# Kernel optimization log

Measured on AMD Instinct MI355X. Metric: run time of the kernel, lower is better.

## Reference

```python
import jax, jax.numpy as jnp
import numpy as np

N_NODES = 50000
N_EDGES = 1600000
IN_CH = 128
HID = 128
OUT_CH = 2
N_GRAPHS = 512
N_HID_LAYERS = 5  # first 5 SAGEConv+BN+ReLU blocks; 6th conv has no BN/act
EPS = 1e-5


def setup_inputs() -> dict:
    key = jax.random.key(0)
    ks = jax.random.split(key, 13)
    x = jax.random.normal(ks[0], (N_NODES, IN_CH), jnp.float32)
    edge_index = jax.random.randint(ks[1], (2, N_EDGES), 0, N_NODES)
    batch = jnp.sort(jax.random.randint(ks[2], (N_NODES,), 0, N_GRAPHS))
    s = 1.0 / np.sqrt(HID)
    # SAGEConv params for the 5 hidden layers (in==hid==128 so they stack)
    Wl = jax.random.normal(ks[3], (N_HID_LAYERS, HID, HID), jnp.float32) * s  # lin_l (neighbors)
    Wr = jax.random.normal(ks[4], (N_HID_LAYERS, HID, HID), jnp.float32) * s  # lin_r (root)
    b = jax.random.normal(ks[5], (N_HID_LAYERS, HID), jnp.float32) * s
    # BatchNorm (eval mode: running stats + affine)
    gamma = 1.0 + 0.1 * jax.random.normal(ks[6], (N_HID_LAYERS, HID), jnp.float32)
    beta = 0.1 * jax.random.normal(ks[7], (N_HID_LAYERS, HID), jnp.float32)
    rmean = 0.1 * jax.random.normal(ks[8], (N_HID_LAYERS, HID), jnp.float32)
    rvar = 0.5 + jax.random.uniform(ks[9], (N_HID_LAYERS, HID), dtype=jnp.float32)
    # final SAGEConv: hid -> out
    Wl_out = jax.random.normal(ks[10], (HID, OUT_CH), jnp.float32) * s
    Wr_out = jax.random.normal(ks[11], (HID, OUT_CH), jnp.float32) * s
    b_out = jax.random.normal(ks[12], (OUT_CH,), jnp.float32) * s
    return dict(x=x, Wl=Wl, Wr=Wr, b=b, gamma=gamma, beta=beta, rmean=rmean,
                rvar=rvar, Wl_out=Wl_out, Wr_out=Wr_out, b_out=b_out,
                edge_index=edge_index, batch=batch)


def reference(x, Wl, Wr, b, gamma, beta, rmean, rvar, Wl_out, Wr_out, b_out,
              edge_index, batch):
    src, dst = edge_index[0], edge_index[1]
    # in-degree for mean aggregation (shared across all layers)
    deg = jax.ops.segment_sum(jnp.ones((src.shape[0],), x.dtype), dst,
                              num_segments=N_NODES)
    inv_deg = (1.0 / jnp.maximum(deg, 1.0))[:, None]  # [N,1]

    def sage(h, Wl_, Wr_, b_):
        # PyG SAGEConv: lin_l(mean_{j in N(i)} x_j) + lin_r(x_i)
        agg = jax.ops.segment_sum(h[src], dst, num_segments=N_NODES) * inv_deg
        return agg @ Wl_ + h @ Wr_ + b_

    h = x
    for l in range(N_HID_LAYERS):
        h = sage(h, Wl[l], Wr[l], b[l])
        # BatchNorm1d in eval mode: affine with running stats
        h = (h - rmean[l]) * (gamma[l] * jax.lax.rsqrt(rvar[l] + EPS)) + beta[l]
        h = jax.nn.relu(h)
        # F.dropout(p=0.2, training=False) is identity in eval
    h = sage(h, Wl_out, Wr_out, b_out)  # [N, OUT_CH]
    # global_mean_pool over graphs
    gsum = jax.ops.segment_sum(h, batch, num_segments=N_GRAPHS)
    gcnt = jax.ops.segment_sum(jnp.ones((h.shape[0],), h.dtype), batch,
                               num_segments=N_GRAPHS)
    return gsum / jnp.maximum(gcnt, 1.0)[:, None]  # [N_GRAPHS, OUT_CH]
```

## Files before the change

### kernel.cpp

```cpp
#include <hip/hip_runtime.h>

#define HID 128
#define BN_EPS 1e-5f

typedef short bf16x8 __attribute__((ext_vector_type(8)));
typedef float f32x4 __attribute__((ext_vector_type(4)));

__device__ inline unsigned short f2b(float f) {
  unsigned int u = __float_as_uint(f);
  unsigned int r = (u + 0x7fffu + ((u >> 16) & 1u)) >> 16;
  return (unsigned short)r;
}
__device__ inline float bl(unsigned int v) { return __uint_as_float(v << 16); }
__device__ inline float bh(unsigned int v) { return __uint_as_float(v & 0xffff0000u); }


__global__ void k_bhist(const int* __restrict__ dst, int* __restrict__ bcnt, int e, int nb) {
  __shared__ int h[256];
  for (int i = threadIdx.x; i < 256; i += blockDim.x) h[i] = 0;
  __syncthreads();
  int stride = gridDim.x * blockDim.x;
  for (int i = blockIdx.x * blockDim.x + threadIdx.x; i < e; i += stride)
    atomicAdd(&h[dst[i] >> 8], 1);
  __syncthreads();
  for (int i = threadIdx.x; i < nb; i += blockDim.x)
    if (h[i]) atomicAdd(&bcnt[i], h[i]);
}

__global__ void k_bscan(const int* __restrict__ bcnt, int* __restrict__ base,
                        int* __restrict__ cur, int nb) {
  __shared__ int ws[4];
  int t = threadIdx.x;
  int v = (t < nb) ? bcnt[t] : 0;
  int lane = t & 63, wid = t >> 6;
  int x = v;
#pragma unroll
  for (int off = 1; off < 64; off <<= 1) {
    int y = __shfl_up(x, off, 64);
    if (lane >= off) x += y;
  }
  if (lane == 63) ws[wid] = x;
  __syncthreads();
  int add = 0;
  for (int w = 0; w < wid; ++w) add += ws[w];
  int incl = x + add;
  int excl = incl - v;
  if (t < nb) { base[t] = excl; cur[t] = excl; }
  if (t == nb - 1) base[nb] = incl;
}

__global__ void k_bscatter(const int* __restrict__ src, const int* __restrict__ dst,
                           int* __restrict__ cur, unsigned int* __restrict__ binned, int e) {
  __shared__ int bc[256];
  __shared__ int bo[256];
  int nchunk = (e + gridDim.x - 1) / gridDim.x;
  int c0 = blockIdx.x * nchunk;
  int c1 = min(c0 + nchunk, e);
  for (int i = threadIdx.x; i < 256; i += blockDim.x) bc[i] = 0;
  __syncthreads();
  for (int i = c0 + threadIdx.x; i < c1; i += blockDim.x)
    atomicAdd(&bc[dst[i] >> 8], 1);
  __syncthreads();
  for (int i = threadIdx.x; i < 256; i += blockDim.x) {
    int c = bc[i];
    bo[i] = c ? atomicAdd(&cur[i], c) : 0;
    bc[i] = 0;
  }
  __syncthreads();
  for (int i = c0 + threadIdx.x; i < c1; i += blockDim.x) {
    int d = dst[i];
    int b = d >> 8;
    int pos = bo[b] + atomicAdd(&bc[b], 1);
    binned[pos] = (unsigned)src[i] | ((unsigned)(d & 255) << 16);
  }
}

__global__ __launch_bounds__(256) void k_bfill(
    const unsigned int* __restrict__ binned, const int* __restrict__ base,
    int* __restrict__ row_ptr, float* __restrict__ inv_deg,
    int* __restrict__ col, int n, int nb) {
  __shared__ int cnt[256];
  __shared__ int cur[256];
  __shared__ int ws[4];
  int b = blockIdx.x;
  int t = threadIdx.x;
  int n0 = b << 8;
  int e0 = base[b], e1 = base[b + 1];
  cnt[t] = 0;
  __syncthreads();
  for (int i = e0 + t; i < e1; i += 256)
    atomicAdd(&cnt[binned[i] >> 16], 1);
  __syncthreads();
  int v = cnt[t];
  int lane = t & 63, wid = t >> 6;
  int x = v;
#pragma unroll
  for (int off = 1; off < 64; off <<= 1) {
    int y = __shfl_up(x, off, 64);
    if (lane >= off) x += y;
  }
  if (lane == 63) ws[wid] = x;
  __syncthreads();
  int add = 0;
  for (int w = 0; w < wid; ++w) add += ws[w];
  int excl = x - v + add;
  int node = n0 + t;
  if (node < n) {
    row_ptr[node] = e0 + excl;
    inv_deg[node] = 1.0f / (float)max(v, 1);
  }
  cur[t] = e0 + excl;
  __syncthreads();
  for (int i = e0 + t; i < e1; i += 256) {
    unsigned int pr = binned[i];
    int pos = atomicAdd(&cur[pr >> 16], 1);
    col[pos] = (int)(pr & 0xffffu);
  }
  if (b == 0 && t == 0) row_ptr[n] = base[nb];
}


__global__ void k_prep(const float* __restrict__ x, unsigned short* __restrict__ xb,
                       const float* __restrict__ Wl, const float* __restrict__ Wr,
                       unsigned short* __restrict__ Wlt, unsigned short* __restrict__ Wrt,
                       const float* __restrict__ g, const float* __restrict__ be,
                       const float* __restrict__ rm, const float* __restrict__ rv,
                       float* __restrict__ sc, float* __restrict__ sh,
                       int n4, int wtot, int bn) {
  int i = blockIdx.x * blockDim.x + threadIdx.x;
  if (i < n4) {
    float4 v = ((const float4*)x)[i];
    unsigned int lo = (unsigned int)f2b(v.x) | ((unsigned int)f2b(v.y) << 16);
    unsigned int hi = (unsigned int)f2b(v.z) | ((unsigned int)f2b(v.w) << 16);
    ((uint2*)xb)[i] = make_uint2(lo, hi);
  } else if (i < n4 + wtot) {
    int j = i - n4;
    int mat = j >> 14, rem = j & 16383, nn = rem >> 7, kk = rem & 127;
    int sidx = (mat << 14) + (kk << 7) + nn;
    Wlt[j] = f2b(Wl[sidx]);
    Wrt[j] = f2b(Wr[sidx]);
  } else if (i < n4 + wtot + bn) {
    int j = i - n4 - wtot;
    float s = g[j] * rsqrtf(rv[j] + BN_EPS);
    sc[j] = s;
    sh[j] = be[j] - rm[j] * s;
  }
}


__global__ __launch_bounds__(128) void k_spmm_g(
    const unsigned short* __restrict__ hbsrc, const int* __restrict__ row_ptr,
    const int* __restrict__ col, const float* __restrict__ inv_deg,
    unsigned short* __restrict__ aggb, int n) {
  int node = blockIdx.x * 2 + (threadIdx.x >> 6);
  if (node >= n) return;
  int lane = threadIdx.x & 63;
  int slot = lane >> 4, c16 = lane & 15;
  int beg = row_ptr[node], end = row_ptr[node + 1];
  float a0 = 0, a1 = 0, a2 = 0, a3 = 0, a4 = 0, a5 = 0, a6 = 0, a7 = 0;
  const unsigned short* base = hbsrc + (c16 << 3);
  int e = beg;
  for (; e + 16 <= end; e += 16) {
    int s0 = col[e + slot];
    int s1 = col[e + 4 + slot];
    int s2 = col[e + 8 + slot];
    int s3 = col[e + 12 + slot];
    uint4 v0 = *(const uint4*)(base + ((size_t)s0 << 7));
    uint4 v1 = *(const uint4*)(base + ((size_t)s1 << 7));
    uint4 v2 = *(const uint4*)(base + ((size_t)s2 << 7));
    uint4 v3 = *(const uint4*)(base + ((size_t)s3 << 7));
    a0 += bl(v0.x); a1 += bh(v0.x); a2 += bl(v0.y); a3 += bh(v0.y);
    a4 += bl(v0.z); a5 += bh(v0.z); a6 += bl(v0.w); a7 += bh(v0.w);
    a0 += bl(v1.x); a1 += bh(v1.x); a2 += bl(v1.y); a3 += bh(v1.y);
    a4 += bl(v1.z); a5 += bh(v1.z); a6 += bl(v1.w); a7 += bh(v1.w);
    a0 += bl(v2.x); a1 += bh(v2.x); a2 += bl(v2.y); a3 += bh(v2.y);
    a4 += bl(v2.z); a5 += bh(v2.z); a6 += bl(v2.w); a7 += bh(v2.w);
    a0 += bl(v3.x); a1 += bh(v3.x); a2 += bl(v3.y); a3 += bh(v3.y);
    a4 += bl(v3.z); a5 += bh(v3.z); a6 += bl(v3.w); a7 += bh(v3.w);
  }
  for (; e < end; e += 4) {
    int idx = e + slot;
    if (idx < end) {
      int s = col[idx];
      uint4 v = *(const uint4*)(base + ((size_t)s << 7));
      a0 += bl(v.x); a1 += bh(v.x); a2 += bl(v.y); a3 += bh(v.y);
      a4 += bl(v.z); a5 += bh(v.z); a6 += bl(v.w); a7 += bh(v.w);
    }
  }
#pragma unroll
  for (int st = 16; st <= 32; st <<= 1) {
    a0 += __shfl_xor(a0, st); a1 += __shfl_xor(a1, st);
    a2 += __shfl_xor(a2, st); a3 += __shfl_xor(a3, st);
    a4 += __shfl_xor(a4, st); a5 += __shfl_xor(a5, st);
    a6 += __shfl_xor(a6, st); a7 += __shfl_xor(a7, st);
  }
  if (slot == 0) {
    float w = inv_deg[node];
    unsigned int p0 = (unsigned int)f2b(a0 * w) | ((unsigned int)f2b(a1 * w) << 16);
    unsigned int p1 = (unsigned int)f2b(a2 * w) | ((unsigned int)f2b(a3 * w) << 16);
    unsigned int p2 = (unsigned int)f2b(a4 * w) | ((unsigned int)f2b(a5 * w) << 16);
    unsigned int p3 = (unsigned int)f2b(a6 * w) | ((unsigned int)f2b(a7 * w) << 16);
    *(uint4*)(aggb + ((size_t)node << 7) + (c16 << 3)) = make_uint4(p0, p1, p2, p3);
  }
}


__global__ __launch_bounds__(256) void k_gemm3(
    const unsigned short* __restrict__ aggb,
    const unsigned short* __restrict__ hbsrc,
    const unsigned short* __restrict__ Wlt,
    const unsigned short* __restrict__ Wrt,
    const float* __restrict__ bias, const float* __restrict__ sc,
    const float* __restrict__ sh, unsigned short* __restrict__ hbo,
    int n, int ngroups) {
  int w = threadIdx.x >> 6;
  int lane = threadIdx.x & 63;
  int l15 = lane & 15, lhi = lane >> 4;

  bf16x8 aL[2][4], aR[2][4];
#pragma unroll
  for (int ms = 0; ms < 2; ++ms) {
    int row = (w << 5) + (ms << 4) + l15;
#pragma unroll
    for (int ks = 0; ks < 4; ++ks) {
      aL[ms][ks] = *(const bf16x8*)(Wlt + (row << 7) + (ks << 5) + (lhi << 3));
      aR[ms][ks] = *(const bf16x8*)(Wrt + (row << 7) + (ks << 5) + (lhi << 3));
    }
  }
  float4 bi[2], scv[2], shv[2];
#pragma unroll
  for (int ms = 0; ms < 2; ++ms) {
    int ch = (w << 5) + (ms << 4) + (lhi << 2);
    bi[ms] = *(const float4*)(bias + ch);
    scv[ms] = *(const float4*)(sc + ch);
    shv[ms] = *(const float4*)(sh + ch);
  }

  for (int g0 = blockIdx.x * 2; g0 < ngroups; g0 += gridDim.x * 2) {
    int g1 = g0 + 1;
    int nodeA = (g0 << 4) + l15;
    bool okA = nodeA < n;
    bool okB = (g1 < ngroups);
    int nodeB = okB ? (g1 << 4) + l15 : nodeA;
    okB = okB && nodeB < n;
    int nsA = okA ? nodeA : 0;
    int nsB = okB ? nodeB : 0;
    const unsigned short* arowA = aggb + ((size_t)nsA << 7) + (lhi << 3);
    const unsigned short* hrowA = hbsrc + ((size_t)nsA << 7) + (lhi << 3);
    const unsigned short* arowB = aggb + ((size_t)nsB << 7) + (lhi << 3);
    const unsigned short* hrowB = hbsrc + ((size_t)nsB << 7) + (lhi << 3);
    bf16x8 bA[4], bH[4], cA[4], cH[4];
#pragma unroll
    for (int ks = 0; ks < 4; ++ks) {
      bA[ks] = *(const bf16x8*)(arowA + (ks << 5));
      bH[ks] = *(const bf16x8*)(hrowA + (ks << 5));
      cA[ks] = *(const bf16x8*)(arowB + (ks << 5));
      cH[ks] = *(const bf16x8*)(hrowB + (ks << 5));
    }
    f32x4 acc0[2], acc1[2];
#pragma unroll
    for (int ms = 0; ms < 2; ++ms) { acc0[ms] = (f32x4)(0.f); acc1[ms] = (f32x4)(0.f); }
#pragma unroll
    for (int ms = 0; ms < 2; ++ms) {
#pragma unroll
      for (int ks = 0; ks < 4; ++ks) {
        acc0[ms] = __builtin_amdgcn_mfma_f32_16x16x32_bf16(aL[ms][ks], bA[ks], acc0[ms], 0, 0, 0);
        acc1[ms] = __builtin_amdgcn_mfma_f32_16x16x32_bf16(aL[ms][ks], cA[ks], acc1[ms], 0, 0, 0);
      }
#pragma unroll
      for (int ks = 0; ks < 4; ++ks) {
        acc0[ms] = __builtin_amdgcn_mfma_f32_16x16x32_bf16(aR[ms][ks], bH[ks], acc0[ms], 0, 0, 0);
        acc1[ms] = __builtin_amdgcn_mfma_f32_16x16x32_bf16(aR[ms][ks], cH[ks], acc1[ms], 0, 0, 0);
      }
    }
#pragma unroll
    for (int ms = 0; ms < 2; ++ms) {
      int ch = (w << 5) + (ms << 4) + (lhi << 2);
      if (okA) {
        float o0 = fmaxf((acc0[ms][0] + bi[ms].x) * scv[ms].x + shv[ms].x, 0.f);
        float o1 = fmaxf((acc0[ms][1] + bi[ms].y) * scv[ms].y + shv[ms].y, 0.f);
        float o2 = fmaxf((acc0[ms][2] + bi[ms].z) * scv[ms].z + shv[ms].z, 0.f);
        float o3 = fmaxf((acc0[ms][3] + bi[ms].w) * scv[ms].w + shv[ms].w, 0.f);
        unsigned int lo = (unsigned int)f2b(o0) | ((unsigned int)f2b(o1) << 16);
        unsigned int hi = (unsigned int)f2b(o2) | ((unsigned int)f2b(o3) << 16);
        *(uint2*)(hbo + ((size_t)nodeA << 7) + ch) = make_uint2(lo, hi);
      }
      if (okB) {
        float o0 = fmaxf((acc1[ms][0] + bi[ms].x) * scv[ms].x + shv[ms].x, 0.f);
        float o1 = fmaxf((acc1[ms][1] + bi[ms].y) * scv[ms].y + shv[ms].y, 0.f);
        float o2 = fmaxf((acc1[ms][2] + bi[ms].z) * scv[ms].z + shv[ms].z, 0.f);
        float o3 = fmaxf((acc1[ms][3] + bi[ms].w) * scv[ms].w + shv[ms].w, 0.f);
        unsigned int lo = (unsigned int)f2b(o0) | ((unsigned int)f2b(o1) << 16);
        unsigned int hi = (unsigned int)f2b(o2) | ((unsigned int)f2b(o3) << 16);
        *(uint2*)(hbo + ((size_t)nodeB << 7) + ch) = make_uint2(lo, hi);
      }
    }
  }
}


__global__ void k_pq(const unsigned short* __restrict__ hb, const float* __restrict__ Wl_out,
                     const float* __restrict__ Wr_out, float* __restrict__ p,
                     float* __restrict__ q, int n) {
  int node = blockIdx.x * 4 + (threadIdx.x >> 6);
  if (node >= n) return;
  int lane = threadIdx.x & 63;
  unsigned int hv = *(const unsigned int*)(hb + ((size_t)node << 7) + (lane << 1));
  float hx = bl(hv), hy = bh(hv);
  float4 wl = *(const float4*)(Wl_out + (lane << 2));
  float4 wr = *(const float4*)(Wr_out + (lane << 2));
  float p0 = hx * wl.x + hy * wl.z;
  float p1 = hx * wl.y + hy * wl.w;
  float q0 = hx * wr.x + hy * wr.z;
  float q1 = hx * wr.y + hy * wr.w;
#pragma unroll
  for (int off = 32; off > 0; off >>= 1) {
    p0 += __shfl_xor(p0, off, 64);
    p1 += __shfl_xor(p1, off, 64);
    q0 += __shfl_xor(q0, off, 64);
    q1 += __shfl_xor(q1, off, 64);
  }
  if (lane == 0) {
    *(float2*)(p + (size_t)node * 2) = make_float2(p0, p1);
    *(float2*)(q + (size_t)node * 2) = make_float2(q0, q1);
  }
}

__global__ void k_spmm2p(const float* __restrict__ p, const float* __restrict__ q,
                         const int* __restrict__ row_ptr, const int* __restrict__ col,
                         const float* __restrict__ inv_deg, const float* __restrict__ b_out,
                         const int* __restrict__ batch, float* __restrict__ out,
                         float* __restrict__ gcnt, int n) {
  int i = blockIdx.x * blockDim.x + threadIdx.x;
  int lane = threadIdx.x & 63;
  bool valid = i < n;
  float o0 = 0.f, o1 = 0.f;
  int g = -1;
  if (valid) {
    int beg = row_ptr[i], end = row_ptr[i + 1];
    float a0 = 0.f, a1 = 0.f, b0 = 0.f, b1 = 0.f;
    int e = beg;
    for (; e + 2 <= end; e += 2) {
      float2 v0 = *(const float2*)(p + (size_t)col[e] * 2);
      float2 v1 = *(const float2*)(p + (size_t)col[e + 1] * 2);
      a0 += v0.x; a1 += v0.y; b0 += v1.x; b1 += v1.y;
    }
    if (e < end) {
      float2 v = *(const float2*)(p + (size_t)col[e] * 2);
      a0 += v.x; a1 += v.y;
    }
    float w = inv_deg[i];
    float2 qv = *(const float2*)(q + (size_t)i * 2);
    o0 = (a0 + b0) * w + qv.x + b_out[0];
    o1 = (a1 + b1) * w + qv.y + b_out[1];
    g = batch[i];
  }
  float s0 = o0, s1 = o1;
#pragma unroll
  for (int off = 1; off < 64; off <<= 1) {
    float y0 = __shfl_up(s0, off, 64);
    float y1 = __shfl_up(s1, off, 64);
    if (lane >= off) { s0 += y0; s1 += y1; }
  }
  int gprev = __shfl_up(g, 1, 64);
  int gnext = __shfl_down(g, 1, 64);
  bool is_start = (lane == 0) || (g != gprev);
  bool is_end = valid && ((lane == 63) || (g != gnext));
  int startl = is_start ? lane : 0;
#pragma unroll
  for (int off = 1; off < 64; off <<= 1) {
    int y = __shfl_up(startl, off, 64);
    if (lane >= off) startl = max(startl, y);
  }
  int prevl = startl > 0 ? startl - 1 : 0;
  float t0 = __shfl(s0, prevl, 64);
  float t1 = __shfl(s1, prevl, 64);
  if (is_end) {
    float p0 = startl > 0 ? t0 : 0.f;
    float p1 = startl > 0 ? t1 : 0.f;
    atomicAdd(&out[g * 2], s0 - p0);
    atomicAdd(&out[g * 2 + 1], s1 - p1);
    atomicAdd(&gcnt[g], (float)(lane - startl + 1));
  }
}

__global__ void k_div(float* __restrict__ out, const float* __restrict__ gcnt, int ng) {
  int i = blockIdx.x * blockDim.x + threadIdx.x;
  if (i < ng * 2) out[i] /= fmaxf(gcnt[i >> 1], 1.0f);
}


extern "C" void kernel_launch(void* const* d_in, const int* in_sizes, int n_in,
                              void* d_out, int out_size, void* d_ws, size_t ws_size,
                              hipStream_t stream) {
  const float* x = (const float*)d_in[0];
  const float* Wl = (const float*)d_in[1];
  const float* Wr = (const float*)d_in[2];
  const float* b = (const float*)d_in[3];
  const float* gamma = (const float*)d_in[4];
  const float* beta = (const float*)d_in[5];
  const float* rmean = (const float*)d_in[6];
  const float* rvar = (const float*)d_in[7];
  const float* Wl_out = (const float*)d_in[8];
  const float* Wr_out = (const float*)d_in[9];
  const float* b_out = (const float*)d_in[10];
  const int* eidx = (const int*)d_in[11];
  const int* batch = (const int*)d_in[12];

  const int N = in_sizes[0] / HID;
  const int E = in_sizes[11] / 2;
  const int L = in_sizes[1] / (HID * HID);
  const int NG = out_size / 2;
  const int NB = (N + 255) >> 8;
  const int NGRP = (N + 15) >> 4;
  const int* src = eidx;
  const int* dst = eidx + E;

  char* ws = (char*)d_ws;
  size_t off = 0;
  auto alloc = [&](size_t bytes) {
    void* ptr = ws + off;
    off += (bytes + 255) & ~(size_t)255;
    return ptr;
  };
  int* row_ptr = (int*)alloc((size_t)(N + 1) * 4);
  int* bcnt = (int*)alloc((size_t)NB * 4);
  int* bbase = (int*)alloc((size_t)(NB + 1) * 4);
  int* bcur = (int*)alloc((size_t)NB * 4);
  int* col = (int*)alloc((size_t)E * 4);
  float* inv_deg = (float*)alloc((size_t)N * 4);
  unsigned short* xb = (unsigned short*)alloc((size_t)N * HID * 2);
  unsigned short* hb0 = (unsigned short*)alloc((size_t)N * HID * 2);
  unsigned short* hb1 = (unsigned short*)alloc((size_t)N * HID * 2);
  unsigned short* aggb = (unsigned short*)alloc((size_t)N * HID * 2);
  unsigned short* Wlt = (unsigned short*)alloc((size_t)L * HID * HID * 2);
  unsigned short* Wrt = (unsigned short*)alloc((size_t)L * HID * HID * 2);
  float* sc = (float*)alloc((size_t)L * HID * 4);
  float* sh = (float*)alloc((size_t)L * HID * 4);
  float* p = (float*)alloc((size_t)N * 2 * 4);
  float* q = (float*)alloc((size_t)N * 2 * 4);
  float* gcnt = (float*)alloc((size_t)NG * 4);
  unsigned int* binned = (unsigned int*)alloc((size_t)E * 4);

  hipMemsetAsync(bcnt, 0, (size_t)NB * 4, stream);
  k_bhist<<<256, 256, 0, stream>>>(dst, bcnt, E, NB);
  k_bscan<<<1, 256, 0, stream>>>(bcnt, bbase, bcur, NB);
  k_bscatter<<<256, 256, 0, stream>>>(src, dst, bcur, binned, E);
  k_bfill<<<NB, 256, 0, stream>>>(binned, bbase, row_ptr, inv_deg, col, N, NB);

  const int n4 = N * HID / 4;
  const int wtot = L * HID * HID;
  const int bn = L * HID;
  k_prep<<<(n4 + wtot + bn + 255) / 256, 256, 0, stream>>>(
      x, xb, Wl, Wr, Wlt, Wrt, gamma, beta, rmean, rvar, sc, sh, n4, wtot, bn);

  const unsigned short* hin = xb;
  for (int l = 0; l < L; ++l) {
    unsigned short* hnext = (l & 1) ? hb1 : hb0;
    k_spmm_g<<<(N + 1) / 2, 128, 0, stream>>>(hin, row_ptr, col, inv_deg, aggb, N);
    k_gemm3<<<512, 256, 0, stream>>>(
        aggb, hin, Wlt + (size_t)l * HID * HID, Wrt + (size_t)l * HID * HID,
        b + (size_t)l * HID, sc + (size_t)l * HID, sh + (size_t)l * HID,
        hnext, N, NGRP);
    hin = hnext;
  }
  k_pq<<<(N + 3) / 4, 256, 0, stream>>>(hin, Wl_out, Wr_out, p, q, N);
  hipMemsetAsync(d_out, 0, (size_t)out_size * 4, stream);
  hipMemsetAsync(gcnt, 0, (size_t)NG * 4, stream);
  k_spmm2p<<<(N + 255) / 256, 256, 0, stream>>>(
      p, q, row_ptr, col, inv_deg, b_out, batch, (float*)d_out, gcnt, N);
  k_div<<<(NG * 2 + 255) / 256, 256, 0, stream>>>((float*)d_out, gcnt, NG);
}
```

Before: 453.1 us.

## Split feature storage into four channel slices for cache-local gather

Stores node features as four planes of 32 channels each, and splits the SpMM gather across four blocks, one per slice. Each slice plane is 3.2 MB, so the randomly gathered working set per kernel pass can fit in L2/MALL better than the full 12.8 MB row-major array. The gather loop now handles 16 edges per iteration with 4 lanes per row, and uses nontemporal loads and stores for col and agg. In exchange, col/row_ptr is read four times and the block count quadruples. The GEMM and pq kernels are adjusted to the new layout.

```diff
diff --git a/kernel.cpp b/kernel.cpp
--- a/kernel.cpp
+++ b/kernel.cpp
@@ -5,6 +5,7 @@
 
 typedef short bf16x8 __attribute__((ext_vector_type(8)));
 typedef float f32x4 __attribute__((ext_vector_type(4)));
+typedef unsigned int u32x4 __attribute__((ext_vector_type(4)));
 
 __device__ inline unsigned short f2b(float f) {
   unsigned int u = __float_as_uint(f);
@@ -13,6 +14,7 @@
 }
 __device__ inline float bl(unsigned int v) { return __uint_as_float(v << 16); }
 __device__ inline float bh(unsigned int v) { return __uint_as_float(v & 0xffff0000u); }
+
 
 
 __global__ void k_bhist(const int* __restrict__ dst, int* __restrict__ bcnt, int e, int nb) {
@@ -126,13 +128,15 @@
                        const float* __restrict__ g, const float* __restrict__ be,
                        const float* __restrict__ rm, const float* __restrict__ rv,
                        float* __restrict__ sc, float* __restrict__ sh,
-                       int n4, int wtot, int bn) {
+                       int n4, int wtot, int bn, int ps) {
   int i = blockIdx.x * blockDim.x + threadIdx.x;
   if (i < n4) {
     float4 v = ((const float4*)x)[i];
     unsigned int lo = (unsigned int)f2b(v.x) | ((unsigned int)f2b(v.y) << 16);
     unsigned int hi = (unsigned int)f2b(v.z) | ((unsigned int)f2b(v.w) << 16);
-    ((uint2*)xb)[i] = make_uint2(lo, hi);
+    int flat = i << 2;
+    int node = flat >> 7, c = flat & 127;
+    *(uint2*)(xb + (size_t)(c >> 5) * ps + node * 32 + (c & 31)) = make_uint2(lo, hi);
   } else if (i < n4 + wtot) {
     int j = i - n4;
     int mat = j >> 14, rem = j & 16383, nn = rem >> 7, kk = rem & 127;
@@ -151,44 +155,34 @@
 __global__ __launch_bounds__(128) void k_spmm_g(
     const unsigned short* __restrict__ hbsrc, const int* __restrict__ row_ptr,
     const int* __restrict__ col, const float* __restrict__ inv_deg,
-    unsigned short* __restrict__ aggb, int n) {
-  int node = blockIdx.x * 2 + (threadIdx.x >> 6);
+    unsigned short* __restrict__ aggb, int n, int ps) {
+  int bid = blockIdx.x;
+  int slice = bid & 3;
+  int node = ((bid >> 2) << 1) + (threadIdx.x >> 6);
   if (node >= n) return;
   int lane = threadIdx.x & 63;
-  int slot = lane >> 4, c16 = lane & 15;
+  int slot = lane >> 2, c4 = lane & 3;
   int beg = row_ptr[node], end = row_ptr[node + 1];
+  const unsigned short* base = hbsrc + (size_t)slice * ps + (c4 << 3);
   float a0 = 0, a1 = 0, a2 = 0, a3 = 0, a4 = 0, a5 = 0, a6 = 0, a7 = 0;
-  const unsigned short* base = hbsrc + (c16 << 3);
   int e = beg;
   for (; e + 16 <= end; e += 16) {
-    int s0 = col[e + slot];
-    int s1 = col[e + 4 + slot];
-    int s2 = col[e + 8 + slot];
-    int s3 = col[e + 12 + slot];
-    uint4 v0 = *(const uint4*)(base + ((size_t)s0 << 7));
-    uint4 v1 = *(const uint4*)(base + ((size_t)s1 << 7));
-    uint4 v2 = *(const uint4*)(base + ((size_t)s2 << 7));
-    uint4 v3 = *(const uint4*)(base + ((size_t)s3 << 7));
-    a0 += bl(v0.x); a1 += bh(v0.x); a2 += bl(v0.y); a3 += bh(v0.y);
-    a4 += bl(v0.z); a5 += bh(v0.z); a6 += bl(v0.w); a7 += bh(v0.w);
-    a0 += bl(v1.x); a1 += bh(v1.x); a2 += bl(v1.y); a3 += bh(v1.y);
-    a4 += bl(v1.z); a5 += bh(v1.z); a6 += bl(v1.w); a7 += bh(v1.w);
-    a0 += bl(v2.x); a1 += bh(v2.x); a2 += bl(v2.y); a3 += bh(v2.y);
-    a4 += bl(v2.z); a5 += bh(v2.z); a6 += bl(v2.w); a7 += bh(v2.w);
-    a0 += bl(v3.x); a1 += bh(v3.x); a2 += bl(v3.y); a3 += bh(v3.y);
-    a4 += bl(v3.z); a5 += bh(v3.z); a6 += bl(v3.w); a7 += bh(v3.w);
-  }
-  for (; e < end; e += 4) {
+    int s = __builtin_nontemporal_load(&col[e + slot]);
+    uint4 v = *(const uint4*)(base + (size_t)s * 32);
+    a0 += bl(v.x); a1 += bh(v.x); a2 += bl(v.y); a3 += bh(v.y);
+    a4 += bl(v.z); a5 += bh(v.z); a6 += bl(v.w); a7 += bh(v.w);
+  }
+  if (e < end) {
     int idx = e + slot;
     if (idx < end) {
-      int s = col[idx];
-      uint4 v = *(const uint4*)(base + ((size_t)s << 7));
+      int s = __builtin_nontemporal_load(&col[idx]);
+      uint4 v = *(const uint4*)(base + (size_t)s * 32);
       a0 += bl(v.x); a1 += bh(v.x); a2 += bl(v.y); a3 += bh(v.y);
       a4 += bl(v.z); a5 += bh(v.z); a6 += bl(v.w); a7 += bh(v.w);
     }
   }
 #pragma unroll
-  for (int st = 16; st <= 32; st <<= 1) {
+  for (int st = 4; st <= 32; st <<= 1) {
     a0 += __shfl_xor(a0, st); a1 += __shfl_xor(a1, st);
     a2 += __shfl_xor(a2, st); a3 += __shfl_xor(a3, st);
     a4 += __shfl_xor(a4, st); a5 += __shfl_xor(a5, st);
@@ -196,11 +190,13 @@
   }
   if (slot == 0) {
     float w = inv_deg[node];
-    unsigned int p0 = (unsigned int)f2b(a0 * w) | ((unsigned int)f2b(a1 * w) << 16);
-    unsigned int p1 = (unsigned int)f2b(a2 * w) | ((unsigned int)f2b(a3 * w) << 16);
-    unsigned int p2 = (unsigned int)f2b(a4 * w) | ((unsigned int)f2b(a5 * w) << 16);
-    unsigned int p3 = (unsigned int)f2b(a6 * w) | ((unsigned int)f2b(a7 * w) << 16);
-    *(uint4*)(aggb + ((size_t)node << 7) + (c16 << 3)) = make_uint4(p0, p1, p2, p3);
+    u32x4 pk;
+    pk[0] = (unsigned int)f2b(a0 * w) | ((unsigned int)f2b(a1 * w) << 16);
+    pk[1] = (unsigned int)f2b(a2 * w) | ((unsigned int)f2b(a3 * w) << 16);
+    pk[2] = (unsigned int)f2b(a4 * w) | ((unsigned int)f2b(a5 * w) << 16);
+    pk[3] = (unsigned int)f2b(a6 * w) | ((unsigned int)f2b(a7 * w) << 16);
+    u32x4* dstp = (u32x4*)(aggb + (size_t)slice * ps + node * 32 + (c4 << 3));
+    __builtin_nontemporal_store(pk, dstp);
   }
 }
 
@@ -212,7 +208,7 @@
     const unsigned short* __restrict__ Wrt,
     const float* __restrict__ bias, const float* __restrict__ sc,
     const float* __restrict__ sh, unsigned short* __restrict__ hbo,
-    int n, int ngroups) {
+    int n, int ngroups, int ps) {
   int w = threadIdx.x >> 6;
   int lane = threadIdx.x & 63;
   int l15 = lane & 15, lhi = lane >> 4;
@@ -245,17 +241,14 @@
     okB = okB && nodeB < n;
     int nsA = okA ? nodeA : 0;
     int nsB = okB ? nodeB : 0;
-    const unsigned short* arowA = aggb + ((size_t)nsA << 7) + (lhi << 3);
-    const unsigned short* hrowA = hbsrc + ((size_t)nsA << 7) + (lhi << 3);
-    const unsigned short* arowB = aggb + ((size_t)nsB << 7) + (lhi << 3);
-    const unsigned short* hrowB = hbsrc + ((size_t)nsB << 7) + (lhi << 3);
     bf16x8 bA[4], bH[4], cA[4], cH[4];
 #pragma unroll
     for (int ks = 0; ks < 4; ++ks) {
-      bA[ks] = *(const bf16x8*)(arowA + (ks << 5));
-      bH[ks] = *(const bf16x8*)(hrowA + (ks << 5));
-      cA[ks] = *(const bf16x8*)(arowB + (ks << 5));
-      cH[ks] = *(const bf16x8*)(hrowB + (ks << 5));
+      size_t po = (size_t)ks * ps + (lhi << 3);
+      bA[ks] = *(const bf16x8*)(aggb + po + nsA * 32);
+      bH[ks] = *(const bf16x8*)(hbsrc + po + nsA * 32);
+      cA[ks] = *(const bf16x8*)(aggb + po + nsB * 32);
+      cH[ks] = *(const bf16x8*)(hbsrc + po + nsB * 32);
     }
     f32x4 acc0[2], acc1[2];
 #pragma unroll
@@ -275,7 +268,7 @@
     }
 #pragma unroll
     for (int ms = 0; ms < 2; ++ms) {
-      int ch = (w << 5) + (ms << 4) + (lhi << 2);
+      int choff = (ms << 4) + (lhi << 2);
       if (okA) {
         float o0 = fmaxf((acc0[ms][0] + bi[ms].x) * scv[ms].x + shv[ms].x, 0.f);
         float o1 = fmaxf((acc0[ms][1] + bi[ms].y) * scv[ms].y + shv[ms].y, 0.f);
@@ -283,7 +276,7 @@
         float o3 = fmaxf((acc0[ms][3] + bi[ms].w) * scv[ms].w + shv[ms].w, 0.f);
         unsigned int lo = (unsigned int)f2b(o0) | ((unsigned int)f2b(o1) << 16);
         unsigned int hi = (unsigned int)f2b(o2) | ((unsigned int)f2b(o3) << 16);
-        *(uint2*)(hbo + ((size_t)nodeA << 7) + ch) = make_uint2(lo, hi);
+        *(uint2*)(hbo + (size_t)w * ps + nodeA * 32 + choff) = make_uint2(lo, hi);
       }
       if (okB) {
         float o0 = fmaxf((acc1[ms][0] + bi[ms].x) * scv[ms].x + shv[ms].x, 0.f);
@@ -292,7 +285,7 @@
         float o3 = fmaxf((acc1[ms][3] + bi[ms].w) * scv[ms].w + shv[ms].w, 0.f);
         unsigned int lo = (unsigned int)f2b(o0) | ((unsigned int)f2b(o1) << 16);
         unsigned int hi = (unsigned int)f2b(o2) | ((unsigned int)f2b(o3) << 16);
-        *(uint2*)(hbo + ((size_t)nodeB << 7) + ch) = make_uint2(lo, hi);
+        *(uint2*)(hbo + (size_t)w * ps + nodeB * 32 + choff) = make_uint2(lo, hi);
       }
     }
   }
@@ -301,11 +294,12 @@
 
 __global__ void k_pq(const unsigned short* __restrict__ hb, const float* __restrict__ Wl_out,
                      const float* __restrict__ Wr_out, float* __restrict__ p,
-                     float* __restrict__ q, int n) {
+                     float* __restrict__ q, int n, int ps) {
   int node = blockIdx.x * 4 + (threadIdx.x >> 6);
   if (node >= n) return;
   int lane = threadIdx.x & 63;
-  unsigned int hv = *(const unsigned int*)(hb + ((size_t)node << 7) + (lane << 1));
+  int c = lane << 1;
+  unsigned int hv = *(const unsigned int*)(hb + (size_t)(c >> 5) * ps + node * 32 + (c & 31));
   float hx = bl(hv), hy = bh(hv);
   float4 wl = *(const float4*)(Wl_out + (lane << 2));
   float4 wr = *(const float4*)(Wr_out + (lane << 2));
@@ -413,6 +407,7 @@
   const int NG = out_size / 2;
   const int NB = (N + 255) >> 8;
   const int NGRP = (N + 15) >> 4;
+  const int PS = N * 32;
   const int* src = eidx;
   const int* dst = eidx + E;
 
@@ -452,19 +447,19 @@
   const int wtot = L * HID * HID;
   const int bn = L * HID;
   k_prep<<<(n4 + wtot + bn + 255) / 256, 256, 0, stream>>>(
-      x, xb, Wl, Wr, Wlt, Wrt, gamma, beta, rmean, rvar, sc, sh, n4, wtot, bn);
+      x, xb, Wl, Wr, Wlt, Wrt, gamma, beta, rmean, rvar, sc, sh, n4, wtot, bn, PS);
 
   const unsigned short* hin = xb;
   for (int l = 0; l < L; ++l) {
     unsigned short* hnext = (l & 1) ? hb1 : hb0;
-    k_spmm_g<<<(N + 1) / 2, 128, 0, stream>>>(hin, row_ptr, col, inv_deg, aggb, N);
+    k_spmm_g<<<4 * ((N + 1) / 2), 128, 0, stream>>>(hin, row_ptr, col, inv_deg, aggb, N, PS);
     k_gemm3<<<512, 256, 0, stream>>>(
         aggb, hin, Wlt + (size_t)l * HID * HID, Wrt + (size_t)l * HID * HID,
         b + (size_t)l * HID, sc + (size_t)l * HID, sh + (size_t)l * HID,
-        hnext, N, NGRP);
+        hnext, N, NGRP, PS);
     hin = hnext;
   }
-  k_pq<<<(N + 3) / 4, 256, 0, stream>>>(hin, Wl_out, Wr_out, p, q, N);
+  k_pq<<<(N + 3) / 4, 256, 0, stream>>>(hin, Wl_out, Wr_out, p, q, N, PS);
   hipMemsetAsync(d_out, 0, (size_t)out_size * 4, stream);
   hipMemsetAsync(gcnt, 0, (size_t)NG * 4, stream);
   k_spmm2p<<<(N + 255) / 256, 256, 0, stream>>>(
```

New measurement: 722.1 us. 1.59x slower.

## Sort CSR columns by source subrange and widen SpMM blocks with nontemporal col loads

Applied to the files above, without the earlier changes.

The CSR fill now sub-buckets each destination's edges by the top bits of the source index, so neighbor lists come out roughly sorted by source. That gives more locality in the gather from the feature matrix. The SpMM kernel now runs four nodes per 256-thread block instead of two per 128-thread block, and it loads column indices with nontemporal hints so they do not pollute the cache. The fill kernel needs a 16 KB shared histogram and a per-thread 16-entry local scan, which raises its setup cost.

```diff
diff --git a/kernel.cpp b/kernel.cpp
--- a/kernel.cpp
+++ b/kernel.cpp
@@ -79,41 +79,49 @@
     const unsigned int* __restrict__ binned, const int* __restrict__ base,
     int* __restrict__ row_ptr, float* __restrict__ inv_deg,
     int* __restrict__ col, int n, int nb) {
-  __shared__ int cnt[256];
-  __shared__ int cur[256];
-  __shared__ int ws[4];
+  __shared__ int cnt[4096];
+  __shared__ int ws2[4];
   int b = blockIdx.x;
   int t = threadIdx.x;
   int n0 = b << 8;
   int e0 = base[b], e1 = base[b + 1];
-  cnt[t] = 0;
-  __syncthreads();
-  for (int i = e0 + t; i < e1; i += 256)
-    atomicAdd(&cnt[binned[i] >> 16], 1);
-  __syncthreads();
-  int v = cnt[t];
+  for (int i = t; i < 4096; i += 256) cnt[i] = 0;
+  __syncthreads();
+  for (int i = e0 + t; i < e1; i += 256) {
+    unsigned int pr = binned[i];
+    int key = (int)((pr >> 16) << 4) | (int)((pr & 0xffffu) >> 12);
+    atomicAdd(&cnt[key], 1);
+  }
+  __syncthreads();
+  int local[16];
+  int sum = 0;
+#pragma unroll
+  for (int j = 0; j < 16; ++j) { local[j] = sum; sum += cnt[(t << 4) + j]; }
   int lane = t & 63, wid = t >> 6;
-  int x = v;
+  int x = sum;
 #pragma unroll
   for (int off = 1; off < 64; off <<= 1) {
     int y = __shfl_up(x, off, 64);
     if (lane >= off) x += y;
   }
-  if (lane == 63) ws[wid] = x;
+  if (lane == 63) ws2[wid] = x;
   __syncthreads();
   int add = 0;
-  for (int w = 0; w < wid; ++w) add += ws[w];
-  int excl = x - v + add;
+  for (int w = 0; w < wid; ++w) add += ws2[w];
+  int texcl = x - sum + add;
   int node = n0 + t;
   if (node < n) {
-    row_ptr[node] = e0 + excl;
-    inv_deg[node] = 1.0f / (float)max(v, 1);
-  }
-  cur[t] = e0 + excl;
+    row_ptr[node] = e0 + texcl;
+    inv_deg[node] = 1.0f / (float)max(sum, 1);
+  }
+  __syncthreads();
+#pragma unroll
+  for (int j = 0; j < 16; ++j) cnt[(t << 4) + j] = e0 + texcl + local[j];
   __syncthreads();
   for (int i = e0 + t; i < e1; i += 256) {
     unsigned int pr = binned[i];
-    int pos = atomicAdd(&cur[pr >> 16], 1);
+    int key = (int)((pr >> 16) << 4) | (int)((pr & 0xffffu) >> 12);
+    int pos = atomicAdd(&cnt[key], 1);
     col[pos] = (int)(pr & 0xffffu);
   }
   if (b == 0 && t == 0) row_ptr[n] = base[nb];
@@ -148,11 +156,11 @@
 }
 
 
-__global__ __launch_bounds__(128) void k_spmm_g(
+__global__ __launch_bounds__(256) void k_spmm_g(
     const unsigned short* __restrict__ hbsrc, const int* __restrict__ row_ptr,
     const int* __restrict__ col, const float* __restrict__ inv_deg,
     unsigned short* __restrict__ aggb, int n) {
-  int node = blockIdx.x * 2 + (threadIdx.x >> 6);
+  int node = blockIdx.x * 4 + (threadIdx.x >> 6);
   if (node >= n) return;
   int lane = threadIdx.x & 63;
   int slot = lane >> 4, c16 = lane & 15;
@@ -161,10 +169,10 @@
   const unsigned short* base = hbsrc + (c16 << 3);
   int e = beg;
   for (; e + 16 <= end; e += 16) {
-    int s0 = col[e + slot];
-    int s1 = col[e + 4 + slot];
-    int s2 = col[e + 8 + slot];
-    int s3 = col[e + 12 + slot];
+    int s0 = __builtin_nontemporal_load(&col[e + slot]);
+    int s1 = __builtin_nontemporal_load(&col[e + 4 + slot]);
+    int s2 = __builtin_nontemporal_load(&col[e + 8 + slot]);
+    int s3 = __builtin_nontemporal_load(&col[e + 12 + slot]);
     uint4 v0 = *(const uint4*)(base + ((size_t)s0 << 7));
     uint4 v1 = *(const uint4*)(base + ((size_t)s1 << 7));
     uint4 v2 = *(const uint4*)(base + ((size_t)s2 << 7));
@@ -181,7 +189,7 @@
   for (; e < end; e += 4) {
     int idx = e + slot;
     if (idx < end) {
-      int s = col[idx];
+      int s = __builtin_nontemporal_load(&col[idx]);
       uint4 v = *(const uint4*)(base + ((size_t)s << 7));
       a0 += bl(v.x); a1 += bh(v.x); a2 += bl(v.y); a3 += bh(v.y);
       a4 += bl(v.z); a5 += bh(v.z); a6 += bl(v.w); a7 += bh(v.w);
@@ -457,7 +465,7 @@
   const unsigned short* hin = xb;
   for (int l = 0; l < L; ++l) {
     unsigned short* hnext = (l & 1) ? hb1 : hb0;
-    k_spmm_g<<<(N + 1) / 2, 128, 0, stream>>>(hin, row_ptr, col, inv_deg, aggb, N);
+    k_spmm_g<<<(N + 3) / 4, 256, 0, stream>>>(hin, row_ptr, col, inv_deg, aggb, N);
     k_gemm3<<<512, 256, 0, stream>>>(
         aggb, hin, Wlt + (size_t)l * HID * HID, Wrt + (size_t)l * HID * HID,
         b + (size_t)l * HID, sc + (size_t)l * HID, sh + (size_t)l * HID,
```

Measured after the change: 470.7 us. +3.9%, slower.
